# Kernel optimization log

Hardware: AMD Instinct MI355X
Metric: run time of the kernel (lower is better)

The kernel has to match this reference:

```python
import jax, jax.numpy as jnp
import numpy as np
from jax import lax

B, C, H, W = 4, 192, 64, 64
D_STATE, D_CONV, EXPAND = 16, 4, 2.0
DI = int(EXPAND * C)           # 384 inner dim
DT_RANK = (C + 15) // 16       # 12
EPS = 1e-5


def setup_inputs() -> dict:
    key = jax.random.key(0)
    ks = jax.random.split(key, 16)
    r = lambda k, shp, s=0.02: jax.random.normal(k, shp, jnp.float32) * s
    inp = {
        'x': jax.random.normal(ks[0], (B, C, H, W), jnp.float32),
        'ln_w': jnp.ones((C,), jnp.float32),
        'ln_b': jnp.zeros((C,), jnp.float32),
        'in_proj_w': r(ks[1], (2 * DI, C)),
        'conv_w': r(ks[2], (DI, 1, D_CONV), 0.1),
        'conv_b': jnp.zeros((DI,), jnp.float32),
        'x_proj_w': r(ks[3], (DT_RANK + 2 * D_STATE, DI)),
        'dt_proj_w': r(ks[4], (DI, DT_RANK), 0.1),
        'dt_proj_b': jnp.full((DI,), -4.0, jnp.float32),  # softplus -> small dt
        'A_log': jnp.log(jnp.broadcast_to(jnp.arange(1, D_STATE + 1, dtype=jnp.float32), (DI, D_STATE))),
        'D': jnp.ones((DI,), jnp.float32),
        'out_proj_w': r(ks[5], (C, DI)),
        'rf_w': r(ks[6], (C, C, 3, 3), 0.05),
        'rf_b': jnp.zeros((C,), jnp.float32),
        'bn_w': jnp.ones((C,), jnp.float32),
        'bn_b': jnp.zeros((C,), jnp.float32),
        'bn_mean': jnp.zeros((C,), jnp.float32),
        'bn_var': jnp.ones((C,), jnp.float32),
    }
    return inp


def _selective_scan(delta, A, Bc, Cc, u):
    # delta,u: (B,L,DI); Bc,Cc: (B,L,N); A: (DI,N)
    def step(h, xs):
        d_t, b_t, c_t, u_t = xs  # (B,DI),(B,N),(B,N),(B,DI)
        dA = jnp.exp(d_t[:, :, None] * A[None])            # (B,DI,N)
        h = dA * h + (d_t * u_t)[:, :, None] * b_t[:, None, :]
        y = jnp.einsum('bdn,bn->bd', h, c_t)
        return h, y
    h0 = jnp.zeros((delta.shape[0], A.shape[0], A.shape[1]), delta.dtype)
    xs = (delta.swapaxes(0, 1), Bc.swapaxes(0, 1), Cc.swapaxes(0, 1), u.swapaxes(0, 1))
    _, ys = lax.scan(step, h0, xs)
    return ys.swapaxes(0, 1)  # (B,L,DI)


def _forward(x, ln_w, ln_b, in_proj_w, conv_w, conv_b, x_proj_w, dt_proj_w,
             dt_proj_b, A_log, D, out_proj_w, rf_w, rf_b, bn_w, bn_b, bn_mean, bn_var):
    b, c, h, w = x.shape
    L = h * w
    t = x.reshape(b, c, L).transpose(0, 2, 1)              # (B,L,C) tokens
    res = t
    mu = t.mean(-1, keepdims=True)
    var = t.var(-1, keepdims=True)
    tn = (t - mu) * lax.rsqrt(var + EPS) * ln_w + ln_b
    xz = jnp.einsum('blc,ec->ble', tn, in_proj_w)          # (B,L,2*DI)
    xi, z = jnp.split(xz, 2, axis=-1)
    # causal depthwise conv1d over L
    xi = xi.transpose(0, 2, 1)                             # (B,DI,L)
    xi = lax.conv_general_dilated(xi, conv_w, (1,), [(D_CONV - 1, 0)],
                                  feature_group_count=DI,
                                  dimension_numbers=('NCH', 'OIH', 'NCH'))
    xi = jax.nn.silu(xi + conv_b[None, :, None])
    xt = xi.transpose(0, 2, 1)                             # (B,L,DI)
    dbl = jnp.einsum('bld,ed->ble', xt, x_proj_w)
    dt, Bc, Cc = jnp.split(dbl, [DT_RANK, DT_RANK + D_STATE], axis=-1)
    delta = jax.nn.softplus(jnp.einsum('blr,dr->bld', dt, dt_proj_w) + dt_proj_b)
    A = -jnp.exp(A_log)
    y = _selective_scan(delta, A, Bc, Cc, xt) + xt * D
    y = y * jax.nn.silu(z)
    t = res + jnp.einsum('bld,cd->blc', y, out_proj_w)     # residual
    x2 = t.transpose(0, 2, 1).reshape(b, c, h, w)
    # refine: conv3x3 + BN(eval) + ReLU
    x2 = lax.conv_general_dilated(x2, rf_w, (1, 1), 'SAME',
                                  dimension_numbers=('NCHW', 'OIHW', 'NCHW'))
    x2 = x2 + rf_b[None, :, None, None]
    x2 = (x2 - bn_mean[None, :, None, None]) * lax.rsqrt(bn_var + EPS)[None, :, None, None]
    x2 = x2 * bn_w[None, :, None, None] + bn_b[None, :, None, None]
    return jax.nn.relu(x2)


def reference(x, ln_w, ln_b, in_proj_w, conv_w, conv_b, x_proj_w, dt_proj_w,
              dt_proj_b, A_log, D, out_proj_w, rf_w, rf_b, bn_w, bn_b, bn_mean, bn_var):
    return _forward(x, ln_w, ln_b, in_proj_w, conv_w, conv_b, x_proj_w, dt_proj_w,
                    dt_proj_b, A_log, D, out_proj_w, rf_w, rf_b, bn_w, bn_b,
                    bn_mean, bn_var)
```

## Files before the change

kernel.cpp:

```cpp
#include <hip/hip_runtime.h>


#define Bn 4
#define Cn 192
#define Hn 64
#define Wn 64
#define Ln 4096
#define DIn 384
#define Nst 16
#define RK 12
#define E2 768
#define NCn 64
#define EPSf 1e-5f

typedef __bf16 bf16x8 __attribute__((ext_vector_type(8)));
typedef float f32x4 __attribute__((ext_vector_type(4)));
typedef unsigned short u16;
typedef unsigned int u32;

static __device__ __forceinline__ float sigmoidf_(float v) {
    return 1.f / (1.f + __expf(-v));
}
static __device__ __forceinline__ float softplusf_(float v) {
    return v > 15.f ? v : __logf(1.f + __expf(v));
}
static __device__ __forceinline__ u16 f2bf(float f) {
    u32 u = __float_as_uint(f);
    u32 r = (u + 0x7FFFu + ((u >> 16) & 1u)) >> 16;
    return (u16)r;
}
static __device__ __forceinline__ float bf2f(u16 v) {
    return __uint_as_float(((u32)v) << 16);
}
static __device__ __forceinline__ float quad_sum_dpp(float p) {
    float a = __int_as_float(__builtin_amdgcn_mov_dpp(__float_as_int(p), 0xB1, 0xF, 0xF, true));
    p += a;
    float b = __int_as_float(__builtin_amdgcn_mov_dpp(__float_as_int(p), 0x4E, 0xF, 0xF, true));
    return p + b;
}
static __device__ __forceinline__ void async16(const u16* g, u16* l) {
    __builtin_amdgcn_global_load_lds((__attribute__((address_space(1))) void*)g,
                                     (__attribute__((address_space(3))) void*)l, 16, 0, 0);
}

__global__ __launch_bounds__(256) void k_prep(const float* __restrict__ rfw,
                                              const float* __restrict__ xpw,
                                              const float* __restrict__ dtw,
                                              const float* __restrict__ inpw,
                                              const float* __restrict__ Wo,
                                              u16* __restrict__ wcv,
                                              u16* __restrict__ wcomb_bf,
                                              u16* __restrict__ inpw_bf,
                                              u16* __restrict__ wo_bf) {
    int g = blockIdx.x * 256 + threadIdx.x;
    if (g < 331776) {
        int tap = g / 36864;
        int rem = g - tap * 36864;
        int co = rem / Cn, ci = rem - co * Cn;
        wcv[g] = f2bf(rfw[((size_t)co * Cn + ci) * 9 + tap]);
    } else if (g < 503808) {
        int i = g - 331776;
        int row = i / 384, k = i - row * 384;
        float v = 0.f;
        if (row < 384) {
#pragma unroll
            for (int r = 0; r < RK; ++r)
                v = fmaf(dtw[row * RK + r], xpw[r * 384 + k], v);
        } else if (row < 416) {
            v = xpw[(RK + row - 384) * 384 + k];
        }
        wcomb_bf[i] = f2bf(v);
    } else if (g < 651264) {
        int i = g - 503808;
        inpw_bf[i] = f2bf(inpw[i]);
    } else if (g < 724992) {
        int i = g - 651264;
        wo_bf[i] = f2bf(Wo[i]);
    }
}

__global__ __launch_bounds__(256) void k_ln(const float* __restrict__ x,
                                            const float* __restrict__ lnw,
                                            const float* __restrict__ lnb,
                                            u16* __restrict__ tn_bf) {
    __shared__ float tile[Cn][65];
    __shared__ float red[2][4][64];
    __shared__ float mean_s[64], rstd_s[64];
    int b = blockIdx.x >> 6;
    int l0 = (blockIdx.x & 63) << 6;
    int tid = threadIdx.x;
    for (int idx = tid; idx < Cn * 64; idx += 256) {
        int c = idx >> 6, ll = idx & 63;
        tile[c][ll] = x[((size_t)(b * Cn + c) << 12) + l0 + ll];
    }
    __syncthreads();
    int ll = tid & 63, grp = tid >> 6;
    float s = 0.f, s2 = 0.f;
    for (int c = grp * 48; c < grp * 48 + 48; ++c) {
        float v = tile[c][ll];
        s += v; s2 += v * v;
    }
    red[0][grp][ll] = s; red[1][grp][ll] = s2;
    __syncthreads();
    if (tid < 64) {
        float m = red[0][0][tid] + red[0][1][tid] + red[0][2][tid] + red[0][3][tid];
        float q = red[1][0][tid] + red[1][1][tid] + red[1][2][tid] + red[1][3][tid];
        m *= (1.f / Cn);
        float var = q * (1.f / Cn) - m * m;
        mean_s[tid] = m;
        rstd_s[tid] = rsqrtf(var + EPSf);
    }
    __syncthreads();
    for (int idx = tid; idx < 64 * Cn; idx += 256) {
        int t = idx / Cn, c = idx - t * Cn;
        float v = (tile[c][t] - mean_s[t]) * rstd_s[t] * lnw[c] + lnb[c];
        tn_bf[(size_t)(b * Ln + l0 + t) * Cn + c] = f2bf(v);
    }
}

template <int K, int KT, int EPI, int NB, int LDO>
__global__ __launch_bounds__(256) void k_gemm3(const u16* __restrict__ A,
                                               const u16* __restrict__ W,
                                               const float* __restrict__ auxf,
                                               const u16* __restrict__ auxb,
                                               void* __restrict__ out1,
                                               float* __restrict__ out2) {
    __shared__ __align__(16) u16 As[2][64 * 64];
    __shared__ __align__(16) u16 Ws[2][64 * 64];
    int bid = blockIdx.x;
    int q = gridDim.x >> 3;
    int wk = (bid & 7) * q + (bid >> 3);
    int n0 = (wk % NB) << 6;
    int m0 = (wk / NB) << 6;
    int tid = threadIdx.x;
    int wid = tid >> 6, lane = tid & 63;
    int lrow = lane & 15, koct = lane >> 4;
    int sw = lrow & 7;
    int i0 = (wid << 7) + lane;
    int r0 = i0 >> 3, g0 = (i0 & 7) ^ (r0 & 7);
    int i1 = i0 + 64;
    int r1 = i1 >> 3, g1 = (i1 & 7) ^ (r1 & 7);
    const u16* a0p = A + (size_t)(m0 + r0) * K + g0 * 8;
    const u16* a1p = A + (size_t)(m0 + r1) * K + g1 * 8;
    const u16* w0p = W + (size_t)(n0 + r0) * K + g0 * 8;
    const u16* w1p = W + (size_t)(n0 + r1) * K + g1 * 8;
    int lb0 = (wid << 7) << 3;
    int lb1 = lb0 + 512;
    f32x4 acc[4];
#pragma unroll
    for (int j = 0; j < 4; ++j) acc[j] = (f32x4){0.f, 0.f, 0.f, 0.f};

    async16(a0p, &As[0][lb0]); async16(a1p, &As[0][lb1]);
    async16(w0p, &Ws[0][lb0]); async16(w1p, &Ws[0][lb1]);
    __syncthreads();
    for (int kt = 0; kt < KT; ++kt) {
        int cur = kt & 1;
        if (kt + 1 < KT) {
            int kk = (kt + 1) << 6;
            async16(a0p + kk, &As[cur ^ 1][lb0]);
            async16(a1p + kk, &As[cur ^ 1][lb1]);
            async16(w0p + kk, &Ws[cur ^ 1][lb0]);
            async16(w1p + kk, &Ws[cur ^ 1][lb1]);
        }
#pragma unroll
        for (int ks = 0; ks < 2; ++ks) {
            int p8 = (((ks << 2) + koct) ^ sw) << 3;
            bf16x8 a  = *(const bf16x8*)&As[cur][(((wid << 4) + lrow) << 6) + p8];
            bf16x8 b0 = *(const bf16x8*)&Ws[cur][(lrow << 6) + p8];
            bf16x8 b1 = *(const bf16x8*)&Ws[cur][((16 + lrow) << 6) + p8];
            bf16x8 b2 = *(const bf16x8*)&Ws[cur][((32 + lrow) << 6) + p8];
            bf16x8 b3 = *(const bf16x8*)&Ws[cur][((48 + lrow) << 6) + p8];
            acc[0] = __builtin_amdgcn_mfma_f32_16x16x32_bf16(a, b0, acc[0], 0, 0, 0);
            acc[1] = __builtin_amdgcn_mfma_f32_16x16x32_bf16(a, b1, acc[1], 0, 0, 0);
            acc[2] = __builtin_amdgcn_mfma_f32_16x16x32_bf16(a, b2, acc[2], 0, 0, 0);
            acc[3] = __builtin_amdgcn_mfma_f32_16x16x32_bf16(a, b3, acc[3], 0, 0, 0);
        }
        __syncthreads();
    }
    int mrow = m0 + (wid << 4) + (koct << 2);
#pragma unroll
    for (int nf = 0; nf < 4; ++nf) {
        int col = n0 + (nf << 4) + lrow;
        if constexpr (EPI == 0) {
            u16* o = (u16*)out1;
#pragma unroll
            for (int r = 0; r < 4; ++r)
                o[(size_t)(mrow + r) * LDO + col] = f2bf(acc[nf][r]);
        } else if constexpr (EPI == 1) {
            if (col < 384) {
                float dtbc = auxf[col];
                u32* dedux = (u32*)out1;
#pragma unroll
                for (int r = 0; r < 4; ++r) {
                    int m = mrow + r;
                    float de = softplusf_(acc[nf][r] + dtbc);
                    float u = bf2f(auxb[(size_t)m * DIn + col]);
                    dedux[(size_t)m * DIn + col] = (u32)f2bf(de) | ((u32)f2bf(de * u) << 16);
                }
            } else if (col < 416) {
#pragma unroll
                for (int r = 0; r < 4; ++r)
                    out2[(size_t)(mrow + r) * 32 + (col - 384)] = acc[nf][r];
            }
        } else {
            u16* t2 = (u16*)out1;
#pragma unroll
            for (int r = 0; r < 4; ++r) {
                int m = mrow + r;
                int b = m >> 12, l = m & 4095;
                float v = acc[nf][r] + auxf[((size_t)(b * Cn + col) << 12) + l];
                t2[(size_t)m * Cn + col] = f2bf(v);
            }
        }
    }
}

__global__ __launch_bounds__(256) void k_conv1d(const u16* __restrict__ xz,
                                                const float* __restrict__ cw,
                                                const float* __restrict__ cb,
                                                u16* __restrict__ xt_bf) {
    int g = blockIdx.x * 256 + threadIdx.x;
    int m = g / 96, dq = g - m * 96;
    int d = dq << 2;
    int l = m & (Ln - 1);
    float w_[4][4];
    *(float4*)&w_[0][0] = *(const float4*)&cw[(d + 0) << 2];
    *(float4*)&w_[1][0] = *(const float4*)&cw[(d + 1) << 2];
    *(float4*)&w_[2][0] = *(const float4*)&cw[(d + 2) << 2];
    *(float4*)&w_[3][0] = *(const float4*)&cw[(d + 3) << 2];
    float4 bv = *(const float4*)&cb[d];
    float o_[4] = {bv.x, bv.y, bv.z, bv.w};
    const u16* base = xz + (size_t)m * E2 + d;
#pragma unroll
    for (int j = 0; j < 4; ++j) {
        if (l >= j) {
            ushort4 in4 = *(const ushort4*)(base - (size_t)j * E2);
            o_[0] += bf2f(in4.x) * w_[0][3 - j];
            o_[1] += bf2f(in4.y) * w_[1][3 - j];
            o_[2] += bf2f(in4.z) * w_[2][3 - j];
            o_[3] += bf2f(in4.w) * w_[3][3 - j];
        }
    }
    ushort4 rb;
    rb.x = f2bf(o_[0] * sigmoidf_(o_[0]));
    rb.y = f2bf(o_[1] * sigmoidf_(o_[1]));
    rb.z = f2bf(o_[2] * sigmoidf_(o_[2]));
    rb.w = f2bf(o_[3] * sigmoidf_(o_[3]));
    *(ushort4*)&xt_bf[(size_t)m * DIn + d] = rb;
}

__global__ __launch_bounds__(256) void k_scan1(const u32* __restrict__ dedux,
                                               const float* __restrict__ bc,
                                               const float* __restrict__ alog,
                                               float* __restrict__ chunkA,
                                               float* __restrict__ chunkH) {
    __shared__ __align__(16) float ds_de[16][20], ds_dux[16][20], ds_bt[16][20];
    int dg = blockIdx.x, c = blockIdx.y, b = blockIdx.z;
    int tid = threadIdx.x;
    int dl = tid >> 4, n = tid & 15;
    int trow = dl, dd = n;
    float Av = -__expf(alog[(dg * 16 + dl) * Nst + n]);
    float h = 0.f, ap = 1.f;
    for (int sub = 0; sub < 4; ++sub) {
        int row = b * Ln + c * 64 + sub * 16 + trow;
        size_t doff = (size_t)row * DIn + dg * 16 + dd;
        u32 v = dedux[doff];
        ds_de[dd][trow] = bf2f((u16)(v & 0xffffu));
        ds_dux[dd][trow] = bf2f((u16)(v >> 16));
        ds_bt[dd][trow] = bc[(size_t)row * 32 + dd];
        __syncthreads();
#pragma unroll
        for (int t4 = 0; t4 < 4; ++t4) {
            f32x4 de4 = *(const f32x4*)&ds_de[dl][t4 * 4];
            f32x4 dux4 = *(const f32x4*)&ds_dux[dl][t4 * 4];
            f32x4 bb4 = *(const f32x4*)&ds_bt[n][t4 * 4];
#pragma unroll
            for (int j = 0; j < 4; ++j) {
                float a = __expf(de4[j] * Av);
                ap *= a;
                h = fmaf(a, h, dux4[j] * bb4[j]);
            }
        }
        __syncthreads();
    }
    size_t base = (size_t)(b * NCn + c) * (DIn * Nst) + dg * 256;
    chunkA[base + tid] = ap;
    chunkH[base + tid] = h;
}

__global__ __launch_bounds__(256) void k_scan15(const float* __restrict__ chunkA,
                                                const float* __restrict__ chunkH,
                                                float* __restrict__ hstart) {
    int dg = blockIdx.x, b = blockIdx.y;
    int tid = threadIdx.x;
    size_t off = (size_t)b * NCn * (DIn * Nst) + dg * 256 + tid;
    float h = 0.f;
    for (int c0 = 0; c0 < NCn; c0 += 8) {
        float Ar[8], Hr[8];
#pragma unroll
        for (int j = 0; j < 8; ++j) {
            Ar[j] = chunkA[off + (size_t)(c0 + j) * (DIn * Nst)];
            Hr[j] = chunkH[off + (size_t)(c0 + j) * (DIn * Nst)];
        }
#pragma unroll
        for (int j = 0; j < 8; ++j) {
            hstart[off + (size_t)(c0 + j) * (DIn * Nst)] = h;
            h = fmaf(Ar[j], h, Hr[j]);
        }
    }
}

__global__ __launch_bounds__(256) void k_scan2(const u32* __restrict__ dedux,
                                               const float* __restrict__ bc,
                                               const float* __restrict__ alog,
                                               const float* __restrict__ hstart,
                                               const u16* __restrict__ xt_bf,
                                               const u16* __restrict__ xz,
                                               const float* __restrict__ Dp,
                                               u16* __restrict__ agate) {
    __shared__ __align__(16) float ds_de[16][20], ds_dux[16][20], ds_bt[16][20], ds_ct[16][20];
    __shared__ __align__(16) float pq[16][16][4];
    int dg = blockIdx.x, c = blockIdx.y, b = blockIdx.z;
    int tid = threadIdx.x;
    int dl = tid >> 4, n = tid & 15;
    int trow = dl, dd = n;
    int aq = n >> 2, bq = n & 3;
    float Av = -__expf(alog[(dg * 16 + dl) * Nst + n]);
    float Dr = Dp[dg * 16 + dd];
    size_t base = (size_t)(b * NCn + c) * (DIn * Nst) + dg * 256;
    float h = hstart[base + tid];
    for (int sub = 0; sub < 4; ++sub) {
        int row = b * Ln + c * 64 + sub * 16 + trow;
        size_t doff = (size_t)row * DIn + dg * 16 + dd;
        u32 v = dedux[doff];
        ds_de[dd][trow] = bf2f((u16)(v & 0xffffu));
        ds_dux[dd][trow] = bf2f((u16)(v >> 16));
        ds_bt[dd][trow] = bc[(size_t)row * 32 + dd];
        ds_ct[dd][trow] = bc[(size_t)row * 32 + 16 + dd];
        float uu = bf2f(xt_bf[doff]);
        float zz = bf2f(xz[(size_t)row * E2 + DIn + dg * 16 + dd]);
        __syncthreads();
        float P[4] = {0.f, 0.f, 0.f, 0.f};
#pragma unroll
        for (int t4 = 0; t4 < 4; ++t4) {
            f32x4 de4 = *(const f32x4*)&ds_de[dl][t4 * 4];
            f32x4 dux4 = *(const f32x4*)&ds_dux[dl][t4 * 4];
            f32x4 bb4 = *(const f32x4*)&ds_bt[n][t4 * 4];
            f32x4 ct4 = *(const f32x4*)&ds_ct[n][t4 * 4];
#pragma unroll
            for (int j = 0; j < 4; ++j) {
                float a = __expf(de4[j] * Av);
                h = fmaf(a, h, dux4[j] * bb4[j]);
                float p = quad_sum_dpp(h * ct4[j]);
                P[t4] = (bq == j) ? p : P[t4];
            }
        }
#pragma unroll
        for (int tt = 0; tt < 4; ++tt)
            pq[tt * 4 + bq][dl][aq] = P[tt];
        __syncthreads();
        f32x4 p4 = *(const f32x4*)&pq[trow][dd][0];
        float y = (p4[0] + p4[1]) + (p4[2] + p4[3]);
        float ga = (y + uu * Dr) * (zz * sigmoidf_(zz));
        agate[doff] = f2bf(ga);
    }
}

__global__ __launch_bounds__(256) void k_conv3(const u16* __restrict__ t2bf,
                                               const u16* __restrict__ wcv,
                                               const float* __restrict__ rfb,
                                               const float* __restrict__ bnw,
                                               const float* __restrict__ bnb,
                                               const float* __restrict__ bnm,
                                               const float* __restrict__ bnv,
                                               float* __restrict__ out) {
    __shared__ __align__(16) u16 in_s[4 * 66 * 40];
    __shared__ __align__(16) u16 w_s[9 * 64 * 40];
    int mt = blockIdx.x;
    int n0 = blockIdx.y << 6;
    int b = mt >> 5;
    int h0 = (mt & 31) << 1;
    int hw0 = h0 << 6;
    int tid = threadIdx.x;
    int wid = tid >> 6, lane = tid & 63;
    int lrow = lane & 15, lk8 = (lane >> 4) << 3, l4 = (lane >> 4) << 2;

    for (int idx = tid; idx < 4 * 40; idx += 256) {
        int rl = idx / 40, k = idx - rl * 40;
        in_s[(rl * 66 + 0) * 40 + k] = 0;
        in_s[(rl * 66 + 65) * 40 + k] = 0;
    }

    int s0 = wid * 32 + lrow;
    int s1 = s0 + 16;
    int abase0 = ((s0 >> 6) * 66 + (s0 & 63)) * 40 + lk8;
    int abase1 = ((s1 >> 6) * 66 + (s1 & 63)) * 40 + lk8;
    int bbase = lrow * 40 + lk8;

    f32x4 acc[2][4];
#pragma unroll
    for (int i = 0; i < 2; ++i)
#pragma unroll
        for (int j = 0; j < 4; ++j) acc[i][j] = (f32x4){0.f, 0.f, 0.f, 0.f};

    int wq = tid >> 2, cq = (tid & 3) << 3;
    for (int ci0 = 0; ci0 < Cn; ci0 += 32) {
        __syncthreads();
#pragma unroll
        for (int rl = 0; rl < 4; ++rl) {
            int gr = h0 - 1 + rl;
            uint4 v = make_uint4(0u, 0u, 0u, 0u);
            if (gr >= 0 && gr < Hn)
                v = *(const uint4*)&t2bf[(size_t)((b << 12) + (gr << 6) + wq) * Cn + ci0 + cq];
            *(uint4*)&in_s[(rl * 66 + wq + 1) * 40 + cq] = v;
        }
#pragma unroll
        for (int tap = 0; tap < 9; ++tap) {
            int co = tid >> 2;
            uint4 v = *(const uint4*)&wcv[((size_t)tap * Cn + n0 + co) * Cn + ci0 + cq];
            *(uint4*)&w_s[(tap * 64 + co) * 40 + cq] = v;
        }
        __syncthreads();
#pragma unroll
        for (int kh = 0; kh < 3; ++kh) {
#pragma unroll
            for (int kw = 0; kw < 3; ++kw) {
                int aoff = (kh * 66 + kw) * 40;
                bf16x8 a0 = *(const bf16x8*)&in_s[abase0 + aoff];
                bf16x8 a1 = *(const bf16x8*)&in_s[abase1 + aoff];
                int boff = (kh * 3 + kw) * 2560;
#pragma unroll
                for (int nf = 0; nf < 4; ++nf) {
                    bf16x8 bb = *(const bf16x8*)&w_s[bbase + nf * 640 + boff];
                    acc[0][nf] = __builtin_amdgcn_mfma_f32_16x16x32_bf16(a0, bb, acc[0][nf], 0, 0, 0);
                    acc[1][nf] = __builtin_amdgcn_mfma_f32_16x16x32_bf16(a1, bb, acc[1][nf], 0, 0, 0);
                }
            }
        }
    }
#pragma unroll
    for (int nf = 0; nf < 4; ++nf) {
        int co = n0 + nf * 16 + lrow;
        float sc = bnw[co] * rsqrtf(bnv[co] + EPSf);
        float sf = (rfb[co] - bnm[co]) * sc + bnb[co];
        size_t obase = ((size_t)(b * Cn + co) << 12) + hw0;
#pragma unroll
        for (int mf = 0; mf < 2; ++mf) {
            int sb = wid * 32 + mf * 16 + l4;
            float4 o;
            o.x = fmaxf(acc[mf][nf][0] * sc + sf, 0.f);
            o.y = fmaxf(acc[mf][nf][1] * sc + sf, 0.f);
            o.z = fmaxf(acc[mf][nf][2] * sc + sf, 0.f);
            o.w = fmaxf(acc[mf][nf][3] * sc + sf, 0.f);
            *(float4*)&out[obase + sb] = o;
        }
    }
}

extern "C" void kernel_launch(void* const* d_in, const int* in_sizes, int n_in,
                              void* d_out, int out_size, void* d_ws, size_t ws_size,
                              hipStream_t stream) {
    const float* x    = (const float*)d_in[0];
    const float* lnw  = (const float*)d_in[1];
    const float* lnb  = (const float*)d_in[2];
    const float* inpw = (const float*)d_in[3];
    const float* cw   = (const float*)d_in[4];
    const float* cb   = (const float*)d_in[5];
    const float* xpw  = (const float*)d_in[6];
    const float* dtw  = (const float*)d_in[7];
    const float* dtb  = (const float*)d_in[8];
    const float* alog = (const float*)d_in[9];
    const float* Dp   = (const float*)d_in[10];
    const float* Wo   = (const float*)d_in[11];
    const float* rfw  = (const float*)d_in[12];
    const float* rfb  = (const float*)d_in[13];
    const float* bnw  = (const float*)d_in[14];
    const float* bnb  = (const float*)d_in[15];
    const float* bnm  = (const float*)d_in[16];
    const float* bnv  = (const float*)d_in[17];

    float* ws = (float*)d_ws;
    u16* tn_bf    = (u16*)ws;
    u16* t2bf     = (u16*)ws;
    float* hstart = ws + 1572864;
    u16* xz       = (u16*)(ws + 3145728);
    u16* xt_bf    = (u16*)(ws + 9437184);
    u32* dedux    = (u32*)(ws + 12582912);
    float* bc     = ws + 18874368;
    u16* agate    = (u16*)(ws + 19398656);
    float* chunkA = ws + 22544384;
    float* chunkH = ws + 24117248;
    u16* wcv      = (u16*)(ws + 25690112);
    u16* wcomb_bf = (u16*)(ws + 25856000);
    u16* inpw_bf  = (u16*)(ws + 25942016);
    u16* wo_bf    = (u16*)(ws + 26015744);

    k_prep<<<2832, 256, 0, stream>>>(rfw, xpw, dtw, inpw, Wo, wcv, wcomb_bf, inpw_bf, wo_bf);
    k_ln<<<Bn * (Ln / 64), 256, 0, stream>>>(x, lnw, lnb, tn_bf);
    k_gemm3<Cn, 3, 0, 12, E2><<<(Bn * Ln / 64) * 12, 256, 0, stream>>>(
        tn_bf, inpw_bf, nullptr, nullptr, xz, nullptr);
    k_conv1d<<<(Bn * Ln * (DIn / 4)) / 256, 256, 0, stream>>>(xz, cw, cb, xt_bf);
    k_gemm3<DIn, 6, 1, 7, 0><<<(Bn * Ln / 64) * 7, 256, 0, stream>>>(
        xt_bf, wcomb_bf, dtb, xt_bf, dedux, bc);
    k_scan1<<<dim3(DIn / 16, NCn, Bn), 256, 0, stream>>>(dedux, bc, alog, chunkA, chunkH);
    k_scan15<<<dim3(DIn / 16, Bn), 256, 0, stream>>>(chunkA, chunkH, hstart);
    k_scan2<<<dim3(DIn / 16, NCn, Bn), 256, 0, stream>>>(dedux, bc, alog, hstart,
                                                         xt_bf, xz, Dp, agate);
    k_gemm3<DIn, 6, 2, 3, Cn><<<(Bn * Ln / 64) * 3, 256, 0, stream>>>(
        agate, wo_bf, x, nullptr, t2bf, nullptr);
    k_conv3<<<dim3(128, Cn / 64), 256, 0, stream>>>(t2bf, wcv, rfb, bnw, bnb, bnm, bnv,
                                                    (float*)d_out);
}
```

Before: 187.1 us.

## Register-prefetch next tiles in scan and conv kernels, use exp2 and sum-of-deltas

The scan kernels and the 3x3 conv kernel now issue global loads for the next sub-chunk or channel slice into registers before the current tile is computed. This lets memory latency overlap with the compute phase. In scan1 the per-step product of decay factors is replaced by exp2 of the summed deltas, and both scans use a native exp2 with a pre-scaled A. The scan2 select is replaced by a mask FMA. The cost is higher register pressure (the conv holds 13 uint4 values), which could lower occupancy.

Result: slower. 205.6 us (+9.9%).

```diff
diff --git a/kernel.cpp b/kernel.cpp
--- a/kernel.cpp
+++ b/kernel.cpp
@@ -31,6 +31,13 @@
 }
 static __device__ __forceinline__ float bf2f(u16 v) {
     return __uint_as_float(((u32)v) << 16);
+}
+static __device__ __forceinline__ float fexp2(float x) {
+#if __has_builtin(__builtin_amdgcn_exp2f)
+    return __builtin_amdgcn_exp2f(x);
+#else
+    return __expf(x * 0.69314718056f);
+#endif
 }
 static __device__ __forceinline__ float quad_sum_dpp(float p) {
     float a = __int_as_float(__builtin_amdgcn_mov_dpp(__float_as_int(p), 0xB1, 0xF, 0xF, true));
@@ -259,16 +266,21 @@
     int tid = threadIdx.x;
     int dl = tid >> 4, n = tid & 15;
     int trow = dl, dd = n;
-    float Av = -__expf(alog[(dg * 16 + dl) * Nst + n]);
-    float h = 0.f, ap = 1.f;
+    float Av2 = -__expf(alog[(dg * 16 + dl) * Nst + n]) * 1.44269504f;
+    float h = 0.f, sde = 0.f;
+    int row0 = b * Ln + c * 64 + trow;
+    u32 vN = dedux[(size_t)row0 * DIn + dg * 16 + dd];
+    float bN = bc[(size_t)row0 * 32 + dd];
     for (int sub = 0; sub < 4; ++sub) {
-        int row = b * Ln + c * 64 + sub * 16 + trow;
-        size_t doff = (size_t)row * DIn + dg * 16 + dd;
-        u32 v = dedux[doff];
-        ds_de[dd][trow] = bf2f((u16)(v & 0xffffu));
-        ds_dux[dd][trow] = bf2f((u16)(v >> 16));
-        ds_bt[dd][trow] = bc[(size_t)row * 32 + dd];
-        __syncthreads();
+        ds_de[dd][trow] = bf2f((u16)(vN & 0xffffu));
+        ds_dux[dd][trow] = bf2f((u16)(vN >> 16));
+        ds_bt[dd][trow] = bN;
+        __syncthreads();
+        if (sub < 3) {
+            int row = row0 + (sub + 1) * 16;
+            vN = dedux[(size_t)row * DIn + dg * 16 + dd];
+            bN = bc[(size_t)row * 32 + dd];
+        }
 #pragma unroll
         for (int t4 = 0; t4 < 4; ++t4) {
             f32x4 de4 = *(const f32x4*)&ds_de[dl][t4 * 4];
@@ -276,15 +288,15 @@
             f32x4 bb4 = *(const f32x4*)&ds_bt[n][t4 * 4];
 #pragma unroll
             for (int j = 0; j < 4; ++j) {
-                float a = __expf(de4[j] * Av);
-                ap *= a;
+                float a = fexp2(de4[j] * Av2);
+                sde += de4[j];
                 h = fmaf(a, h, dux4[j] * bb4[j]);
             }
         }
         __syncthreads();
     }
     size_t base = (size_t)(b * NCn + c) * (DIn * Nst) + dg * 256;
-    chunkA[base + tid] = ap;
+    chunkA[base + tid] = fexp2(Av2 * sde);
     chunkH[base + tid] = h;
 }
 
@@ -325,21 +337,36 @@
     int dl = tid >> 4, n = tid & 15;
     int trow = dl, dd = n;
     int aq = n >> 2, bq = n & 3;
-    float Av = -__expf(alog[(dg * 16 + dl) * Nst + n]);
+    float Av2 = -__expf(alog[(dg * 16 + dl) * Nst + n]) * 1.44269504f;
     float Dr = Dp[dg * 16 + dd];
+    float msk[4];
+#pragma unroll
+    for (int j = 0; j < 4; ++j) msk[j] = (bq == j) ? 1.f : 0.f;
     size_t base = (size_t)(b * NCn + c) * (DIn * Nst) + dg * 256;
     float h = hstart[base + tid];
+    int row0 = b * Ln + c * 64 + trow;
+    u32 vN = dedux[(size_t)row0 * DIn + dg * 16 + dd];
+    float bN = bc[(size_t)row0 * 32 + dd];
+    float cN = bc[(size_t)row0 * 32 + 16 + dd];
+    u16 uN = xt_bf[(size_t)row0 * DIn + dg * 16 + dd];
+    u16 zN = xz[(size_t)row0 * E2 + DIn + dg * 16 + dd];
     for (int sub = 0; sub < 4; ++sub) {
-        int row = b * Ln + c * 64 + sub * 16 + trow;
+        int row = row0 + sub * 16;
         size_t doff = (size_t)row * DIn + dg * 16 + dd;
-        u32 v = dedux[doff];
-        ds_de[dd][trow] = bf2f((u16)(v & 0xffffu));
-        ds_dux[dd][trow] = bf2f((u16)(v >> 16));
-        ds_bt[dd][trow] = bc[(size_t)row * 32 + dd];
-        ds_ct[dd][trow] = bc[(size_t)row * 32 + 16 + dd];
-        float uu = bf2f(xt_bf[doff]);
-        float zz = bf2f(xz[(size_t)row * E2 + DIn + dg * 16 + dd]);
-        __syncthreads();
+        ds_de[dd][trow] = bf2f((u16)(vN & 0xffffu));
+        ds_dux[dd][trow] = bf2f((u16)(vN >> 16));
+        ds_bt[dd][trow] = bN;
+        ds_ct[dd][trow] = cN;
+        float uu = bf2f(uN), zz = bf2f(zN);
+        __syncthreads();
+        if (sub < 3) {
+            int rown = row0 + (sub + 1) * 16;
+            vN = dedux[(size_t)rown * DIn + dg * 16 + dd];
+            bN = bc[(size_t)rown * 32 + dd];
+            cN = bc[(size_t)rown * 32 + 16 + dd];
+            uN = xt_bf[(size_t)rown * DIn + dg * 16 + dd];
+            zN = xz[(size_t)rown * E2 + DIn + dg * 16 + dd];
+        }
         float P[4] = {0.f, 0.f, 0.f, 0.f};
 #pragma unroll
         for (int t4 = 0; t4 < 4; ++t4) {
@@ -349,10 +376,10 @@
             f32x4 ct4 = *(const f32x4*)&ds_ct[n][t4 * 4];
 #pragma unroll
             for (int j = 0; j < 4; ++j) {
-                float a = __expf(de4[j] * Av);
+                float a = fexp2(de4[j] * Av2);
                 h = fmaf(a, h, dux4[j] * bb4[j]);
                 float p = quad_sum_dpp(h * ct4[j]);
-                P[t4] = (bq == j) ? p : P[t4];
+                P[t4] = fmaf(msk[j], p, P[t4]);
             }
         }
 #pragma unroll
@@ -404,23 +431,39 @@
         for (int j = 0; j < 4; ++j) acc[i][j] = (f32x4){0.f, 0.f, 0.f, 0.f};
 
     int wq = tid >> 2, cq = (tid & 3) << 3;
+    uint4 rin[4], rw[9];
+#pragma unroll
+    for (int rl = 0; rl < 4; ++rl) {
+        int gr = h0 - 1 + rl;
+        rin[rl] = make_uint4(0u, 0u, 0u, 0u);
+        if (gr >= 0 && gr < Hn)
+            rin[rl] = *(const uint4*)&t2bf[(size_t)((b << 12) + (gr << 6) + wq) * Cn + cq];
+    }
+#pragma unroll
+    for (int tap = 0; tap < 9; ++tap)
+        rw[tap] = *(const uint4*)&wcv[((size_t)tap * Cn + n0 + wq) * Cn + cq];
+
     for (int ci0 = 0; ci0 < Cn; ci0 += 32) {
-        __syncthreads();
-#pragma unroll
-        for (int rl = 0; rl < 4; ++rl) {
-            int gr = h0 - 1 + rl;
-            uint4 v = make_uint4(0u, 0u, 0u, 0u);
-            if (gr >= 0 && gr < Hn)
-                v = *(const uint4*)&t2bf[(size_t)((b << 12) + (gr << 6) + wq) * Cn + ci0 + cq];
-            *(uint4*)&in_s[(rl * 66 + wq + 1) * 40 + cq] = v;
-        }
-#pragma unroll
-        for (int tap = 0; tap < 9; ++tap) {
-            int co = tid >> 2;
-            uint4 v = *(const uint4*)&wcv[((size_t)tap * Cn + n0 + co) * Cn + ci0 + cq];
-            *(uint4*)&w_s[(tap * 64 + co) * 40 + cq] = v;
-        }
-        __syncthreads();
+#pragma unroll
+        for (int rl = 0; rl < 4; ++rl)
+            *(uint4*)&in_s[(rl * 66 + wq + 1) * 40 + cq] = rin[rl];
+#pragma unroll
+        for (int tap = 0; tap < 9; ++tap)
+            *(uint4*)&w_s[(tap * 64 + wq) * 40 + cq] = rw[tap];
+        __syncthreads();
+        if (ci0 + 32 < Cn) {
+            int cin = ci0 + 32;
+#pragma unroll
+            for (int rl = 0; rl < 4; ++rl) {
+                int gr = h0 - 1 + rl;
+                rin[rl] = make_uint4(0u, 0u, 0u, 0u);
+                if (gr >= 0 && gr < Hn)
+                    rin[rl] = *(const uint4*)&t2bf[(size_t)((b << 12) + (gr << 6) + wq) * Cn + cin + cq];
+            }
+#pragma unroll
+            for (int tap = 0; tap < 9; ++tap)
+                rw[tap] = *(const uint4*)&wcv[((size_t)tap * Cn + n0 + wq) * Cn + cin + cq];
+        }
 #pragma unroll
         for (int kh = 0; kh < 3; ++kh) {
 #pragma unroll
@@ -437,6 +480,7 @@
                 }
             }
         }
+        __syncthreads();
     }
 #pragma unroll
     for (int nf = 0; nf < 4; ++nf) {
```
